# Optimization experiments

Hardware: AMD Instinct MI355X
Metric: run time of the kernel (lower is better)

Reference implementation:

```python
import jax, jax.numpy as jnp
import numpy as np

N = 512          # N_ROIs (nodes)
E = N * N        # number of edges
V = 6            # number of views (edge_attr dim)
DIMS = [(1, 36), (36, 24), (24, 5)]  # (in, out) per NNConv layer


def _nnconv(x, edge_attr, src, dst, We, be, root, bias, cin, cout):
    # edge MLP: Linear + ReLU -> per-edge weight matrix [E, cin, cout]
    w = jax.nn.relu(edge_attr @ We + be).reshape(-1, cin, cout)
    msg = jnp.einsum('ei,eio->eo', x[src], w)              # gather + per-edge matmul
    s = jax.ops.segment_sum(msg, dst, num_segments=N)      # scatter-sum
    cnt = jax.ops.segment_sum(jnp.ones((msg.shape[0], 1), x.dtype), dst, num_segments=N)
    agg = s / jnp.maximum(cnt, 1.0)                        # mean aggregation
    return agg + x @ root + bias                           # root weight + bias (PyG NNConv)


def setup_inputs() -> dict:
    key = jax.random.key(0)
    ks = jax.random.split(key, 16)
    x = jnp.ones((N, 1), jnp.float32)
    edge_attr = jax.random.uniform(ks[0], (E, V), jnp.float32)
    edge_index = jax.random.randint(ks[1], (2, E), 0, N, dtype=jnp.int32)
    inp = {'x': x, 'edge_attr': edge_attr, 'edge_index': edge_index}
    for l, (cin, cout) in enumerate(DIMS, start=1):
        k = jax.random.split(ks[1 + l], 4)
        inp[f'We{l}'] = jax.random.normal(k[0], (V, cin * cout), jnp.float32) / np.sqrt(V)
        inp[f'be{l}'] = jnp.zeros((cin * cout,), jnp.float32)
        inp[f'root{l}'] = jax.random.normal(k[1], (cin, cout), jnp.float32) / np.sqrt(cin)
        inp[f'b{l}'] = jnp.zeros((cout,), jnp.float32)
    return inp


def reference(x, edge_attr, edge_index,
              We1, be1, root1, b1,
              We2, be2, root2, b2,
              We3, be3, root3, b3):
    src, dst = edge_index[0], edge_index[1]
    h = jax.nn.relu(_nnconv(x, edge_attr, src, dst, We1, be1, root1, b1, *DIMS[0]))
    h = jax.nn.relu(_nnconv(h, edge_attr, src, dst, We2, be2, root2, b2, *DIMS[1]))
    h = jax.nn.relu(_nnconv(h, edge_attr, src, dst, We3, be3, root3, b3, *DIMS[2]))
    # pairwise CBT: sum_k |h_i,k - h_j,k|  ->  [N, N]
    cbt = jnp.sum(jnp.abs(h[:, None, :] - h[None, :, :]), axis=2)
    return cbt
```

## Files before the change

kernel.cpp:

```cpp
#include <hip/hip_runtime.h>
#include <hip/hip_bf16.h>

#define N_NODES 512
#define N_EDGES (512 * 512)
#define NBLK 256
#define EPB (N_EDGES / NBLK)

typedef __attribute__((ext_vector_type(2))) _Float16 half2v;

#if defined(__has_builtin)
#if __has_builtin(__builtin_amdgcn_fdot2)
#define FDOT2(a, b, c) __builtin_amdgcn_fdot2((a), (b), (c), false)
#endif
#endif
#ifndef FDOT2
static __device__ inline float fdot2_sw(half2v a, half2v b, float c) {
    return (float)a.x * (float)b.x + (float)a.y * (float)b.y + c;
}
#define FDOT2(a, b, c) fdot2_sw((a), (b), (c))
#endif

static __device__ inline unsigned pack_h2(float x, float y) {
    union { _Float16 h[2]; unsigned u; } c;
    c.h[0] = (_Float16)x;
    c.h[1] = (_Float16)y;
    return c.u;
}
static __device__ inline half2v bits_h2(int b) {
    union { int i; half2v h; } c;
    c.i = b;
    return c.h;
}

__global__ __launch_bounds__(256) void count_kernel(const int* __restrict__ dst,
                                                    int* __restrict__ bcnt) {
    __shared__ int h[N_NODES];
    int tid = threadIdx.x;
    int b = blockIdx.x;
    h[tid] = 0;
    h[tid + 256] = 0;
    __syncthreads();
#pragma unroll
    for (int k = 0; k < EPB / 256; k++)
        atomicAdd(&h[dst[b * EPB + k * 256 + tid]], 1);
    __syncthreads();
    bcnt[b * N_NODES + tid] = h[tid];
    bcnt[b * N_NODES + tid + 256] = h[tid + 256];
}

__global__ __launch_bounds__(512) void scan_kernel(const int* __restrict__ bcnt,
                                                   int* __restrict__ offs,
                                                   int* __restrict__ base) {
    __shared__ int buf[N_NODES];
    int t = threadIdx.x;
    int sum = 0;
    for (int b = 0; b < NBLK; b++) sum += bcnt[b * N_NODES + t];
    buf[t] = sum;
    __syncthreads();
    for (int d = 1; d < N_NODES; d <<= 1) {
        int add = (t >= d) ? buf[t - d] : 0;
        __syncthreads();
        buf[t] += add;
        __syncthreads();
    }
    offs[t + 1] = buf[t];
    if (t == 0) offs[0] = 0;
    int run = buf[t] - sum;
    for (int b = 0; b < NBLK; b++) {
        base[b * N_NODES + t] = run;
        run += bcnt[b * N_NODES + t];
    }
}

__global__ __launch_bounds__(256) void scatter_kernel(const int* __restrict__ src,
                                                      const int* __restrict__ dst,
                                                      const float* __restrict__ ea,
                                                      const int* __restrict__ base,
                                                      int4* __restrict__ ed4) {
    __shared__ int lcur[N_NODES];
    int tid = threadIdx.x;
    int b = blockIdx.x;
    lcur[tid] = base[b * N_NODES + tid];
    lcur[tid + 256] = base[b * N_NODES + tid + 256];
    __syncthreads();
#pragma unroll
    for (int k = 0; k < EPB / 256; k++) {
        int e = b * EPB + k * 256 + tid;
        const float* a = ea + (size_t)e * 6;
        float a0 = a[0], a1 = a[1], a2 = a[2], a3 = a[3], a4 = a[4], a5 = a[5];
        int p = atomicAdd(&lcur[dst[e]], 1);
        int4 r;
        r.x = (int)pack_h2(a0, a1);
        r.y = (int)pack_h2(a2, a3);
        r.z = (int)pack_h2(a4, a5);
        r.w = src[e];
        ed4[p] = r;
    }
}

template <int CIN, int COUT, int OG, int BLK, int G>
__global__ __launch_bounds__(BLK) void nnconv_edges(
    const float* __restrict__ hprev,
    const int4* __restrict__ ed4,
    const int* __restrict__ offs,
    const float* __restrict__ We,
    const float* __restrict__ be,
    float* __restrict__ agg)
{
    constexpr int J = CIN * COUT;
    constexpr int OPL = COUT / OG;
    constexpr int A = CIN * OPL;

    const int n = blockIdx.x / G;
    const int g = blockIdx.x % G;
    const int tid = threadIdx.x;
    const bool act = (tid < A);
    const int i = act ? tid / OPL : 0;
    const int og = act ? (tid % OPL) * OG : 0;

    half2v wrp[OG][3];
    float ber[OG], acc[OG];
#pragma unroll
    for (int k = 0; k < OG; k++) {
        acc[k] = 0.f;
        int j = i * COUT + og + k;
        if (act) {
            ber[k] = be[j];
#pragma unroll
            for (int t = 0; t < 3; t++)
                wrp[k][t] = bits_h2((int)pack_h2(We[(2 * t) * J + j], We[(2 * t + 1) * J + j]));
        } else {
            ber[k] = 0.f;
#pragma unroll
            for (int t = 0; t < 3; t++) wrp[k][t] = bits_h2(0);
        }
    }

    const int start = offs[n];
    const int end = offs[n + 1];
    const int len = end - start;
    const int per = (len + G - 1) / G;
    int p = start + g * per;
    int p1 = p + per;
    if (p1 > end) p1 = end;

    const float* hp_i = hprev + i;

    for (; p + 8 <= p1; p += 8) {
        const int4* eb = ed4 + p;
        int4 ed[8];
#pragma unroll
        for (int u = 0; u < 8; u++) ed[u] = eb[u];
        float xv[8];
#pragma unroll
        for (int u = 0; u < 8; u++) xv[u] = hp_i[ed[u].w * CIN];
#pragma unroll
        for (int u = 0; u < 8; u++) {
            half2v e01 = bits_h2(ed[u].x), e23 = bits_h2(ed[u].y), e45 = bits_h2(ed[u].z);
#pragma unroll
            for (int k = 0; k < OG; k++) {
                float z = FDOT2(e45, wrp[k][2],
                        FDOT2(e23, wrp[k][1],
                        FDOT2(e01, wrp[k][0], ber[k])));
                acc[k] = fmaf(xv[u], fmaxf(z, 0.f), acc[k]);
            }
        }
    }
    for (; p < p1; ++p) {
        int4 ed = ed4[p];
        float xv = hp_i[ed.w * CIN];
        half2v e01 = bits_h2(ed.x), e23 = bits_h2(ed.y), e45 = bits_h2(ed.z);
#pragma unroll
        for (int k = 0; k < OG; k++) {
            float z = FDOT2(e45, wrp[k][2],
                    FDOT2(e23, wrp[k][1],
                    FDOT2(e01, wrp[k][0], ber[k])));
            acc[k] = fmaf(xv, fmaxf(z, 0.f), acc[k]);
        }
    }

    if constexpr (CIN == 1) {
        if (act) atomicAdd(&agg[n * COUT + og], acc[0]);
    } else {
        __shared__ float lds_acc[J];
        if (act) {
#pragma unroll
            for (int k = 0; k < OG; k++) lds_acc[i * COUT + og + k] = acc[k];
        }
        __syncthreads();
        if (tid < COUT) {
            float sum = 0.f;
#pragma unroll
            for (int ii = 0; ii < CIN; ii++) sum += lds_acc[ii * COUT + tid];
            atomicAdd(&agg[n * COUT + tid], sum);
        }
    }
}

template <int CIN, int COUT>
__global__ __launch_bounds__(64) void nnconv_fin(const float* __restrict__ agg,
                                                 const int* __restrict__ offs,
                                                 const float* __restrict__ hprev,
                                                 const float* __restrict__ root,
                                                 const float* __restrict__ bias,
                                                 float* __restrict__ hout) {
    int n = blockIdx.x;
    int t = threadIdx.x;
    if (t >= COUT) return;
    int cnt = offs[n + 1] - offs[n];
    float inv = 1.f / fmaxf((float)cnt, 1.f);
    float v = agg[n * COUT + t] * inv;
#pragma unroll
    for (int i = 0; i < CIN; i++) v = fmaf(hprev[n * CIN + i], root[i * COUT + t], v);
    v += bias[t];
    hout[n * COUT + t] = fmaxf(v, 0.f);
}

__global__ __launch_bounds__(256) void cbt_kernel(const float* __restrict__ h3,
                                                  float* __restrict__ out) {
    __shared__ float lh[N_NODES * 5];
    int tid = threadIdx.x;
    for (int idx = tid; idx < N_NODES * 5; idx += 256) lh[idx] = h3[idx];
    __syncthreads();
    int i = blockIdx.x;
    float hi[5];
#pragma unroll
    for (int k = 0; k < 5; k++) hi[k] = lh[i * 5 + k];
    for (int j = tid; j < N_NODES; j += 256) {
        float sacc = 0.f;
#pragma unroll
        for (int k = 0; k < 5; k++) sacc += fabsf(hi[k] - lh[j * 5 + k]);
        out[i * N_NODES + j] = sacc;
    }
}

extern "C" void kernel_launch(void* const* d_in, const int* in_sizes, int n_in,
                              void* d_out, int out_size, void* d_ws, size_t ws_size,
                              hipStream_t stream) {
    const float* x = (const float*)d_in[0];
    const float* edge_attr = (const float*)d_in[1];
    const int* edge_index = (const int*)d_in[2];
    const float* We1 = (const float*)d_in[3];
    const float* be1 = (const float*)d_in[4];
    const float* root1 = (const float*)d_in[5];
    const float* b1 = (const float*)d_in[6];
    const float* We2 = (const float*)d_in[7];
    const float* be2 = (const float*)d_in[8];
    const float* root2 = (const float*)d_in[9];
    const float* b2 = (const float*)d_in[10];
    const float* We3 = (const float*)d_in[11];
    const float* be3 = (const float*)d_in[12];
    const float* root3 = (const float*)d_in[13];
    const float* b3 = (const float*)d_in[14];

    const int E = N_EDGES;
    const int* src = edge_index;
    const int* dst = edge_index + E;

    char* ws = (char*)d_ws;
    int* offs = (int*)(ws + 0);
    int* bcnt = (int*)(ws + 4096);
    int* base = (int*)(ws + 528384);
    int4* ed4 = (int4*)(ws + 1052672);
    float* agg1 = (float*)(ws + 5246976);
    float* agg2 = (float*)(ws + 5320704);
    float* agg3 = (float*)(ws + 5369856);
    float* h1 = (float*)(ws + 5380096);
    float* h2 = (float*)(ws + 5453824);
    float* h3 = (float*)(ws + 5502976);

    hipMemsetAsync(agg1, 0, 5380096 - 5246976, stream);

    count_kernel<<<NBLK, 256, 0, stream>>>(dst, bcnt);
    scan_kernel<<<1, 512, 0, stream>>>(bcnt, offs, base);
    scatter_kernel<<<NBLK, 256, 0, stream>>>(src, dst, edge_attr, base, ed4);

    nnconv_edges<1, 36, 1, 64, 16><<<N_NODES * 16, 64, 0, stream>>>(x, ed4, offs, We1, be1, agg1);
    nnconv_fin<1, 36><<<N_NODES, 64, 0, stream>>>(agg1, offs, x, root1, b1, h1);

    nnconv_edges<36, 24, 4, 256, 8><<<N_NODES * 8, 256, 0, stream>>>(h1, ed4, offs, We2, be2, agg2);
    nnconv_fin<36, 24><<<N_NODES, 64, 0, stream>>>(agg2, offs, h1, root2, b2, h2);

    nnconv_edges<24, 5, 1, 128, 8><<<N_NODES * 8, 128, 0, stream>>>(h2, ed4, offs, We3, be3, agg3);
    nnconv_fin<24, 5><<<N_NODES, 64, 0, stream>>>(agg3, offs, h2, root3, b3, h3);

    cbt_kernel<<<N_NODES, 256, 0, stream>>>(h3, (float*)d_out);
}
```

Before: 205.2 us.

## Parallelize CSR scan across blocks and double-buffer edge loads in NNConv

The single-block scan, which serially walked 256 block counts per node twice, is split into a per-node column scan kernel launched with 512 blocks plus a small offsets scan. The scatter kernel now adds global offsets to the per-block prefixes itself. The edge loop is restructured from 8-wide batches into 4-wide double-buffered loads so the next edges load while the current ones compute. The src index is masked to stay in bounds, and an inline-asm dot2 fallback is added. The extra kernel launch adds overhead, and the smaller unroll may expose less memory-level parallelism.

After: 197.0 us. 1.04x faster.

```diff
diff --git a/kernel.cpp b/kernel.cpp
--- a/kernel.cpp
+++ b/kernel.cpp
@@ -14,10 +14,12 @@
 #endif
 #endif
 #ifndef FDOT2
-static __device__ inline float fdot2_sw(half2v a, half2v b, float c) {
-    return (float)a.x * (float)b.x + (float)a.y * (float)b.y + c;
-}
-#define FDOT2(a, b, c) fdot2_sw((a), (b), (c))
+static __device__ inline float fdot2_asm(half2v a, half2v b, float c) {
+    float d;
+    asm("v_dot2_f32_f16 %0, %1, %2, %3" : "=v"(d) : "v"(a), "v"(b), "v"(c));
+    return d;
+}
+#define FDOT2(a, b, c) fdot2_asm((a), (b), (c))
 #endif
 
 static __device__ inline unsigned pack_h2(float x, float y) {
@@ -48,14 +50,31 @@
     bcnt[b * N_NODES + tid + 256] = h[tid + 256];
 }
 
-__global__ __launch_bounds__(512) void scan_kernel(const int* __restrict__ bcnt,
-                                                   int* __restrict__ offs,
-                                                   int* __restrict__ base) {
+__global__ __launch_bounds__(NBLK) void colscan_kernel(const int* __restrict__ bcnt,
+                                                       int* __restrict__ pre,
+                                                       int* __restrict__ tot) {
+    __shared__ int buf[NBLK];
+    int t = blockIdx.x;
+    int b = threadIdx.x;
+    int v = bcnt[b * N_NODES + t];
+    buf[b] = v;
+    __syncthreads();
+    for (int d = 1; d < NBLK; d <<= 1) {
+        int add = (b >= d) ? buf[b - d] : 0;
+        __syncthreads();
+        buf[b] += add;
+        __syncthreads();
+    }
+    pre[b * N_NODES + t] = buf[b] - v;
+    if (b == NBLK - 1) tot[t] = buf[b];
+}
+
+__global__ __launch_bounds__(512) void offs_kernel(const int* __restrict__ tot,
+                                                   int* __restrict__ offs) {
     __shared__ int buf[N_NODES];
     int t = threadIdx.x;
-    int sum = 0;
-    for (int b = 0; b < NBLK; b++) sum += bcnt[b * N_NODES + t];
-    buf[t] = sum;
+    int v = tot[t];
+    buf[t] = v;
     __syncthreads();
     for (int d = 1; d < N_NODES; d <<= 1) {
         int add = (t >= d) ? buf[t - d] : 0;
@@ -65,23 +84,19 @@
     }
     offs[t + 1] = buf[t];
     if (t == 0) offs[0] = 0;
-    int run = buf[t] - sum;
-    for (int b = 0; b < NBLK; b++) {
-        base[b * N_NODES + t] = run;
-        run += bcnt[b * N_NODES + t];
-    }
 }
 
 __global__ __launch_bounds__(256) void scatter_kernel(const int* __restrict__ src,
                                                       const int* __restrict__ dst,
                                                       const float* __restrict__ ea,
-                                                      const int* __restrict__ base,
+                                                      const int* __restrict__ pre,
+                                                      const int* __restrict__ offs,
                                                       int4* __restrict__ ed4) {
     __shared__ int lcur[N_NODES];
     int tid = threadIdx.x;
     int b = blockIdx.x;
-    lcur[tid] = base[b * N_NODES + tid];
-    lcur[tid + 256] = base[b * N_NODES + tid + 256];
+    lcur[tid] = offs[tid] + pre[b * N_NODES + tid];
+    lcur[tid + 256] = offs[tid + 256] + pre[b * N_NODES + tid + 256];
     __syncthreads();
 #pragma unroll
     for (int k = 0; k < EPB / 256; k++) {
@@ -144,18 +159,13 @@
     int p1 = p + per;
     if (p1 > end) p1 = end;
 
-    const float* hp_i = hprev + i;
-
-    for (; p + 8 <= p1; p += 8) {
-        const int4* eb = ed4 + p;
-        int4 ed[8];
-#pragma unroll
-        for (int u = 0; u < 8; u++) ed[u] = eb[u];
-        float xv[8];
-#pragma unroll
-        for (int u = 0; u < 8; u++) xv[u] = hp_i[ed[u].w * CIN];
-#pragma unroll
-        for (int u = 0; u < 8; u++) {
+    auto proc4 = [&](const int4* ed) {
+        float xv[4];
+#pragma unroll
+        for (int u = 0; u < 4; u++)
+            xv[u] = hprev[(ed[u].w & (N_NODES - 1)) * CIN + i];
+#pragma unroll
+        for (int u = 0; u < 4; u++) {
             half2v e01 = bits_h2(ed[u].x), e23 = bits_h2(ed[u].y), e45 = bits_h2(ed[u].z);
 #pragma unroll
             for (int k = 0; k < OG; k++) {
@@ -165,10 +175,37 @@
                 acc[k] = fmaf(xv[u], fmaxf(z, 0.f), acc[k]);
             }
         }
-    }
-    for (; p < p1; ++p) {
-        int4 ed = ed4[p];
-        float xv = hp_i[ed.w * CIN];
+    };
+
+    const int nb = (p1 - p) >> 2;
+    {
+        const int4* ep = ed4 + p;
+        int4 bufA[4], bufB[4];
+        if (nb > 0) {
+#pragma unroll
+            for (int u = 0; u < 4; u++) bufA[u] = ep[u];
+            int b = 0;
+            while (b + 2 <= nb) {
+#pragma unroll
+                for (int u = 0; u < 4; u++) bufB[u] = ep[4 + u];
+                proc4(bufA);
+                ep += 4; ++b;
+                if (b + 2 <= nb) {
+#pragma unroll
+                    for (int u = 0; u < 4; u++) bufA[u] = ep[4 + u];
+                    proc4(bufB);
+                    ep += 4; ++b;
+                } else {
+                    proc4(bufB);
+                    ep += 4; ++b;
+                }
+            }
+            if (b < nb) proc4(bufA);
+        }
+    }
+    for (int q = p + (nb << 2); q < p1; ++q) {
+        int4 ed = ed4[q];
+        float xv = hprev[(ed.w & (N_NODES - 1)) * CIN + i];
         half2v e01 = bits_h2(ed.x), e23 = bits_h2(ed.y), e45 = bits_h2(ed.z);
 #pragma unroll
         for (int k = 0; k < OG; k++) {
@@ -260,8 +297,9 @@
     char* ws = (char*)d_ws;
     int* offs = (int*)(ws + 0);
     int* bcnt = (int*)(ws + 4096);
-    int* base = (int*)(ws + 528384);
+    int* pre = (int*)(ws + 528384);
     int4* ed4 = (int4*)(ws + 1052672);
+    int* tot = (int*)(ws + 1052672);
     float* agg1 = (float*)(ws + 5246976);
     float* agg2 = (float*)(ws + 5320704);
     float* agg3 = (float*)(ws + 5369856);
@@ -272,8 +310,9 @@
     hipMemsetAsync(agg1, 0, 5380096 - 5246976, stream);
 
     count_kernel<<<NBLK, 256, 0, stream>>>(dst, bcnt);
-    scan_kernel<<<1, 512, 0, stream>>>(bcnt, offs, base);
-    scatter_kernel<<<NBLK, 256, 0, stream>>>(src, dst, edge_attr, base, ed4);
+    colscan_kernel<<<N_NODES, NBLK, 0, stream>>>(bcnt, pre, tot);
+    offs_kernel<<<1, 512, 0, stream>>>(tot, offs);
+    scatter_kernel<<<NBLK, 256, 0, stream>>>(src, dst, edge_attr, pre, offs, ed4);
 
     nnconv_edges<1, 36, 1, 64, 16><<<N_NODES * 16, 64, 0, stream>>>(x, ed4, offs, We1, be1, agg1);
     nnconv_fin<1, 36><<<N_NODES, 64, 0, stream>>>(agg1, offs, x, root1, b1, h1);
```
